# Performance work log

Hardware: AMD Instinct MI355X
Metric: run time of the kernel (lower is better)

Reference implementation:

```python
import jax, jax.numpy as jnp
import numpy as np

B, N, A, IN_DIM, OUT_DIM, D_OBS = 4096, 16, 8, 128, 128, 128


def setup_inputs() -> dict:
    key = jax.random.key(0)
    k1, k2, k3, k4, k5, k6 = jax.random.split(key, 6)
    h = jax.random.normal(k1, (B, N, IN_DIM), dtype=jnp.float32)
    policies = jax.random.uniform(k2, (B, N, A), dtype=jnp.float32)
    actions = jax.random.uniform(k3, (B, N, A), dtype=jnp.float32)
    obs_proc = jax.random.normal(k4, (B * N, D_OBS), dtype=jnp.float32)
    # xavier-normal-ish params (exact init values irrelevant for correctness baseline)
    W_fc = jax.random.normal(k5, (OUT_DIM, IN_DIM), dtype=jnp.float32) * (2.0 / (IN_DIM + OUT_DIM)) ** 0.5
    W_attn = jax.random.normal(k6, (1, 2 * OUT_DIM), dtype=jnp.float32) * (2.0 / (2 * OUT_DIM + 1)) ** 0.5
    return {"h": h, "policies": policies, "actions": actions, "obs_proc": obs_proc,
            "W_fc": W_fc, "W_attn": W_attn}


def reference(h, policies, actions, obs_proc, W_fc, W_attn):
    # h: [B, N, in_dim]; policies/actions: [B, N, A]; obs_proc: [B*N, D]
    b, n, a = policies.shape
    z = jnp.einsum('bni,oi->bno', h, W_fc)                    # fc(h), [B, N, out]
    out_dim = z.shape[-1]
    # attn_fc(cat[z_src, z_dst]) split into src/dst contributions
    a_src = z @ W_attn[0, :out_dim]                           # [B, N]
    a_dst = z @ W_attn[0, out_dim:]                           # [B, N]
    # e[b, i(dst), j(src)] = leaky_relu(a_src[b,j] + a_dst[b,i])
    e = jax.nn.leaky_relu(a_src[:, None, :] + a_dst[:, :, None], 0.01)
    w = jax.nn.sigmoid(e)[..., None]                          # [B, N(dst), N(src), 1]
    # gated mix of source action / source policy per (dst, src) pair
    zgate = w * actions[:, None, :, :] + (1.0 - w) * policies[:, None, :, :]  # [B,i,j,A]
    # repeat + place_policies/place_zs masked sum + mean over src dim collapses to:
    # out_z[b,i,k] = (sum_j zgate[b,i,j] - zgate[b,i,k] + policies[b,k]) / N
    sum_z = zgate.sum(axis=2)                                 # [B, i, A]
    out_z = (sum_z[:, :, None, :] - zgate + policies[:, None, :, :]) / n  # [B,i,k,A]
    obs_b = obs_proc.reshape(b, n, -1)                        # [B, k, D]
    d = obs_b.shape[-1]
    obs_rep = jnp.broadcast_to(obs_b[:, None, :, :], (b, n, n, d))  # [B, i, k, D]
    obs_final = jnp.concatenate([obs_rep, out_z], axis=-1).reshape(b * n, n, d + a)
    return obs_final, w.reshape(b * n, n, 1)
```

## Files before the change

kernel.cpp:

```cpp
#include <hip/hip_runtime.h>
#include <math.h>

#define B_SZ 4096
#define N_SZ 16
#define A_SZ 8
#define IN_DIM 128
#define OUT_DIM 128
#define D_OBS 128
#define ROW_OUT (D_OBS + A_SZ)

typedef float f32x4 __attribute__((ext_vector_type(4)));

__global__ __launch_bounds__(256) void prep_v(const float* __restrict__ W_fc,
                                              const float* __restrict__ W_attn,
                                              float* __restrict__ v) {
  __shared__ float part[2][2][128];
  const int i = threadIdx.x & 127;
  const int half = threadIdx.x >> 7;
  float s = 0.f, d = 0.f;
  #pragma unroll 8
  for (int oo = 0; oo < 64; ++oo) {
    const int o = half * 64 + oo;
    const float w = W_fc[o * IN_DIM + i];
    s += w * W_attn[o];
    d += w * W_attn[OUT_DIM + o];
  }
  part[half][0][i] = s;
  part[half][1][i] = d;
  __syncthreads();
  if (half == 0) {
    v[i]          = part[0][0][i] + part[1][0][i];
    v[IN_DIM + i] = part[0][1][i] + part[1][1][i];
  }
}

__global__ __launch_bounds__(256) void gat_main(
    const float* __restrict__ h,
    const float* __restrict__ pol,
    const float* __restrict__ act,
    const float* __restrict__ obs,
    const float* __restrict__ v,
    float* __restrict__ out_obs,
    float* __restrict__ out_w)
{
  const int b = blockIdx.x;
  const int tid = threadIdx.x;

  __shared__ float a_src_sm[16];
  __shared__ float a_dst_sm[16];
  __shared__ float w_sm[256];
  __shared__ float pol_sm[128];
  __shared__ float act_sm[128];
  __shared__ float sumz_sm[128];
  __shared__ float outz_sm[2048];
  __shared__ float obs_sm[2048];

  {
    const f32x4* op = (const f32x4*)(obs + (size_t)b * (N_SZ * D_OBS));
    f32x4* od = (f32x4*)obs_sm;
    od[tid]       = __builtin_nontemporal_load(&op[tid]);
    od[tid + 256] = __builtin_nontemporal_load(&op[tid + 256]);
  }
  if (tid < 128) {
    pol_sm[tid] = __builtin_nontemporal_load(&pol[(size_t)b * (N_SZ * A_SZ) + tid]);
    act_sm[tid] = __builtin_nontemporal_load(&act[(size_t)b * (N_SZ * A_SZ) + tid]);
  }

  {
    const int n = tid >> 4;
    const int l = tid & 15;
    const f32x4* hp = (const f32x4*)(h + (size_t)b * (N_SZ * IN_DIM));
    const f32x4 h0 = __builtin_nontemporal_load(&hp[tid * 2]);
    const f32x4 h1 = __builtin_nontemporal_load(&hp[tid * 2 + 1]);
    const f32x4* vs = (const f32x4*)v;
    const f32x4* vd = (const f32x4*)(v + IN_DIM);
    const f32x4 s0 = vs[l * 2], s1 = vs[l * 2 + 1];
    const f32x4 d0 = vd[l * 2], d1 = vd[l * 2 + 1];
    float s = h0.x * s0.x + h0.y * s0.y + h0.z * s0.z + h0.w * s0.w
            + h1.x * s1.x + h1.y * s1.y + h1.z * s1.z + h1.w * s1.w;
    float d = h0.x * d0.x + h0.y * d0.y + h0.z * d0.z + h0.w * d0.w
            + h1.x * d1.x + h1.y * d1.y + h1.z * d1.z + h1.w * d1.w;
    for (int m = 8; m >= 1; m >>= 1) {
      s += __shfl_xor(s, m, 16);
      d += __shfl_xor(d, m, 16);
    }
    if (l == 0) {
      a_src_sm[n] = s;
      a_dst_sm[n] = d;
    }
  }
  __syncthreads();

  {
    const int i = tid >> 4, j = tid & 15;
    float e = a_src_sm[j] + a_dst_sm[i];
    e = (e >= 0.f) ? e : 0.01f * e;
    const float wv = 1.f / (1.f + expf(-e));
    w_sm[tid] = wv;
    __builtin_nontemporal_store(wv, &out_w[(size_t)b * 256 + tid]);
  }
  __syncthreads();

  if (tid < 128) {
    const int i = tid >> 3, a = tid & 7;
    float s = 0.f;
    for (int j = 0; j < N_SZ; ++j) {
      const float wv = w_sm[i * 16 + j];
      s += wv * act_sm[j * 8 + a] + (1.f - wv) * pol_sm[j * 8 + a];
    }
    sumz_sm[tid] = s;
  }
  __syncthreads();

  {
    const int i = tid >> 4, k = tid & 15;
    const float wv = w_sm[tid];
    for (int a = 0; a < A_SZ; ++a) {
      const float zg = wv * act_sm[k * 8 + a] + (1.f - wv) * pol_sm[k * 8 + a];
      outz_sm[tid * 8 + a] =
          (sumz_sm[i * 8 + a] - zg + pol_sm[k * 8 + a]) * 0.0625f;
    }
  }
  __syncthreads();

  float* ob = out_obs + (size_t)b * (256 * ROW_OUT);
  const f32x4* obs4 = (const f32x4*)obs_sm;
  #pragma unroll 2
  for (int idx = tid; idx < 256 * 34; idx += 256) {
    const int r = idx / 34;
    const int d4 = idx - r * 34;
    f32x4 o4;
    if (d4 < 32) {
      const int k = r & 15;
      o4 = obs4[k * 32 + d4];
    } else {
      o4 = *(const f32x4*)(outz_sm + r * 8 + (d4 - 32) * 4);
    }
    __builtin_nontemporal_store(o4, (f32x4*)(ob + (size_t)idx * 4));
  }
}

extern "C" void kernel_launch(void* const* d_in, const int* in_sizes, int n_in,
                              void* d_out, int out_size, void* d_ws, size_t ws_size,
                              hipStream_t stream) {
  const float* h      = (const float*)d_in[0];
  const float* pol    = (const float*)d_in[1];
  const float* act    = (const float*)d_in[2];
  const float* obs    = (const float*)d_in[3];
  const float* W_fc   = (const float*)d_in[4];
  const float* W_attn = (const float*)d_in[5];

  float* out = (float*)d_out;
  float* out_w = out + (size_t)B_SZ * N_SZ * N_SZ * ROW_OUT;
  float* v = (float*)d_ws;

  prep_v<<<1, 256, 0, stream>>>(W_fc, W_attn, v);
  gat_main<<<B_SZ, 256, 0, stream>>>(h, pol, act, obs, v, out, out_w);
}
```

Before: 138.8 us.

## Widen prep kernel, remap block order, use normal stores and incremental indexing

```diff
diff --git a/kernel.cpp b/kernel.cpp
--- a/kernel.cpp
+++ b/kernel.cpp
@@ -11,26 +11,29 @@
 
 typedef float f32x4 __attribute__((ext_vector_type(4)));
 
-__global__ __launch_bounds__(256) void prep_v(const float* __restrict__ W_fc,
-                                              const float* __restrict__ W_attn,
-                                              float* __restrict__ v) {
-  __shared__ float part[2][2][128];
+__global__ __launch_bounds__(1024) void prep_v(const float* __restrict__ W_fc,
+                                               const float* __restrict__ W_attn,
+                                               float* __restrict__ v) {
+  __shared__ float part[8][2][128];
   const int i = threadIdx.x & 127;
-  const int half = threadIdx.x >> 7;
+  const int seg = threadIdx.x >> 7;
   float s = 0.f, d = 0.f;
-  #pragma unroll 8
-  for (int oo = 0; oo < 64; ++oo) {
-    const int o = half * 64 + oo;
+  #pragma unroll
+  for (int oo = 0; oo < 16; ++oo) {
+    const int o = seg * 16 + oo;
     const float w = W_fc[o * IN_DIM + i];
     s += w * W_attn[o];
     d += w * W_attn[OUT_DIM + o];
   }
-  part[half][0][i] = s;
-  part[half][1][i] = d;
+  part[seg][0][i] = s;
+  part[seg][1][i] = d;
   __syncthreads();
-  if (half == 0) {
-    v[i]          = part[0][0][i] + part[1][0][i];
-    v[IN_DIM + i] = part[0][1][i] + part[1][1][i];
+  if (seg == 0) {
+    float ss = 0.f, dd = 0.f;
+    #pragma unroll
+    for (int t = 0; t < 8; ++t) { ss += part[t][0][i]; dd += part[t][1][i]; }
+    v[i] = ss;
+    v[IN_DIM + i] = dd;
   }
 }
 
@@ -43,7 +46,7 @@
     float* __restrict__ out_obs,
     float* __restrict__ out_w)
 {
-  const int b = blockIdx.x;
+  const int b = ((blockIdx.x & 7) << 9) | (blockIdx.x >> 3);
   const int tid = threadIdx.x;
 
   __shared__ float a_src_sm[16];
@@ -67,7 +70,6 @@
   }
 
   {
-    const int n = tid >> 4;
     const int l = tid & 15;
     const f32x4* hp = (const f32x4*)(h + (size_t)b * (N_SZ * IN_DIM));
     const f32x4 h0 = __builtin_nontemporal_load(&hp[tid * 2]);
@@ -85,25 +87,25 @@
       d += __shfl_xor(d, m, 16);
     }
     if (l == 0) {
-      a_src_sm[n] = s;
-      a_dst_sm[n] = d;
+      a_src_sm[tid >> 4] = s;
+      a_dst_sm[tid >> 4] = d;
     }
   }
   __syncthreads();
 
   {
-    const int i = tid >> 4, j = tid & 15;
-    float e = a_src_sm[j] + a_dst_sm[i];
+    float e = a_src_sm[tid & 15] + a_dst_sm[tid >> 4];
     e = (e >= 0.f) ? e : 0.01f * e;
     const float wv = 1.f / (1.f + expf(-e));
     w_sm[tid] = wv;
-    __builtin_nontemporal_store(wv, &out_w[(size_t)b * 256 + tid]);
+    out_w[(size_t)b * 256 + tid] = wv;
   }
   __syncthreads();
 
   if (tid < 128) {
     const int i = tid >> 3, a = tid & 7;
     float s = 0.f;
+    #pragma unroll
     for (int j = 0; j < N_SZ; ++j) {
       const float wv = w_sm[i * 16 + j];
       s += wv * act_sm[j * 8 + a] + (1.f - wv) * pol_sm[j * 8 + a];
@@ -115,6 +117,7 @@
   {
     const int i = tid >> 4, k = tid & 15;
     const float wv = w_sm[tid];
+    #pragma unroll
     for (int a = 0; a < A_SZ; ++a) {
       const float zg = wv * act_sm[k * 8 + a] + (1.f - wv) * pol_sm[k * 8 + a];
       outz_sm[tid * 8 + a] =
@@ -125,18 +128,21 @@
 
   float* ob = out_obs + (size_t)b * (256 * ROW_OUT);
   const f32x4* obs4 = (const f32x4*)obs_sm;
-  #pragma unroll 2
-  for (int idx = tid; idx < 256 * 34; idx += 256) {
-    const int r = idx / 34;
-    const int d4 = idx - r * 34;
-    f32x4 o4;
-    if (d4 < 32) {
-      const int k = r & 15;
-      o4 = obs4[k * 32 + d4];
-    } else {
-      o4 = *(const f32x4*)(outz_sm + r * 8 + (d4 - 32) * 4);
+  {
+    int r  = tid / 34;
+    int d4 = tid - r * 34;
+    #pragma unroll 2
+    for (int idx = tid; idx < 256 * 34; idx += 256) {
+      f32x4 o4;
+      if (d4 < 32) {
+        o4 = obs4[(r & 15) * 32 + d4];
+      } else {
+        o4 = *(const f32x4*)(outz_sm + r * 8 + (d4 - 32) * 4);
+      }
+      *(f32x4*)(ob + (size_t)idx * 4) = o4;
+      r += 7; d4 += 18;
+      if (d4 >= 34) { d4 -= 34; ++r; }
     }
-    __builtin_nontemporal_store(o4, (f32x4*)(ob + (size_t)idx * 4));
   }
 }
 
@@ -154,6 +160,6 @@
   float* out_w = out + (size_t)B_SZ * N_SZ * N_SZ * ROW_OUT;
   float* v = (float*)d_ws;
 
-  prep_v<<<1, 256, 0, stream>>>(W_fc, W_attn, v);
+  prep_v<<<1, 1024, 0, stream>>>(W_fc, W_attn, v);
   gat_main<<<B_SZ, 256, 0, stream>>>(h, pol, act, obs, v, out, out_w);
 }
```

New measurement: 138.5 us. Within noise of the previous version (-0.2%).
